# Performance work log

Measured on AMD Instinct MI355X. Metric: run time of the kernel, lower is better.

The kernel has to match this reference:

```python
import jax, jax.numpy as jnp
import numpy as np

B, CIN, H, W = 4, 1024, 64, 64
PLANES = 256
K = 3
DIL = 2
PAD = DIL * (K - 1) // 2  # = 2
EPS = 1e-5


def setup_inputs() -> dict:
    key = jax.random.key(0)
    ks = jax.random.split(key, 16)
    d = {}
    d['x'] = jax.random.normal(ks[0], (B, CIN, H, W), dtype=jnp.float32)
    # conv1: 1x1, inplanes->planes, no bias
    d['w1'] = jax.random.normal(ks[1], (PLANES, CIN), dtype=jnp.float32) * 0.02
    d['gamma1'] = jnp.ones((PLANES,), jnp.float32)
    d['beta1'] = jnp.zeros((PLANES,), jnp.float32)
    d['mean1'] = jax.random.normal(ks[2], (PLANES,), dtype=jnp.float32) * 0.1
    d['var1'] = jax.random.uniform(ks[3], (PLANES,), minval=0.5, maxval=1.5, dtype=jnp.float32)
    # deform_offset: 3x3 conv planes->18, with bias
    d['woff'] = jax.random.normal(ks[4], (18, PLANES, K, K), dtype=jnp.float32) * 0.01
    d['boff'] = jnp.zeros((18,), jnp.float32)
    # conv2 (deformable): 3x3 planes->planes, with bias
    d['w2'] = jax.random.normal(ks[5], (PLANES, PLANES, K, K), dtype=jnp.float32) * 0.02
    d['bconv2'] = jnp.zeros((PLANES,), jnp.float32)
    d['gamma2'] = jnp.ones((PLANES,), jnp.float32)
    d['beta2'] = jnp.zeros((PLANES,), jnp.float32)
    d['mean2'] = jax.random.normal(ks[6], (PLANES,), dtype=jnp.float32) * 0.1
    d['var2'] = jax.random.uniform(ks[7], (PLANES,), minval=0.5, maxval=1.5, dtype=jnp.float32)
    # conv3: 1x1 planes->planes*4, no bias
    d['w3'] = jax.random.normal(ks[8], (PLANES * 4, PLANES), dtype=jnp.float32) * 0.02
    d['gamma3'] = jnp.ones((PLANES * 4,), jnp.float32)
    d['beta3'] = jnp.zeros((PLANES * 4,), jnp.float32)
    d['mean3'] = jax.random.normal(ks[9], (PLANES * 4,), dtype=jnp.float32) * 0.1
    d['var3'] = jax.random.uniform(ks[10], (PLANES * 4,), minval=0.5, maxval=1.5, dtype=jnp.float32)
    return d


def _bn(x, gamma, beta, mean, var):
    # inference-mode BatchNorm over channel dim (NCHW)
    inv = jax.lax.rsqrt(var + EPS)
    return (x - mean[:, None, None]) * (inv * gamma)[:, None, None] + beta[:, None, None]


def _deform_conv(x, offset, w, b):
    # x: [B,C,H,W]; offset: [B,18,H,W] ordered (dy,dx) per kernel tap; w: [O,C,3,3]
    Bn, C, Hh, Ww = x.shape
    off = offset.reshape(Bn, K * K, 2, Hh, Ww)
    off_y, off_x = off[:, :, 0], off[:, :, 1]          # [B,9,H,W]
    kk = jnp.arange(K * K)
    base_y = (kk // K) * DIL - PAD                      # [9]
    base_x = (kk % K) * DIL - PAD
    ys = jnp.arange(Hh, dtype=x.dtype)
    xs = jnp.arange(Ww, dtype=x.dtype)
    py = base_y.astype(x.dtype)[None, :, None, None] + ys[None, None, :, None] + off_y
    px = base_x.astype(x.dtype)[None, :, None, None] + xs[None, None, None, :] + off_x

    def sample_one(img, py1, px1):
        # img [C,H,W]; py1/px1 [9,H,W] -> [C,9,H,W] bilinear with zero padding
        y0 = jnp.floor(py1)
        x0 = jnp.floor(px1)
        wy = py1 - y0
        wx = px1 - x0

        def gather(yc, xc):
            yi = yc.astype(jnp.int32)
            xi = xc.astype(jnp.int32)
            valid = ((yi >= 0) & (yi < Hh) & (xi >= 0) & (xi < Ww)).astype(img.dtype)
            yi = jnp.clip(yi, 0, Hh - 1)
            xi = jnp.clip(xi, 0, Ww - 1)
            return img[:, yi, xi] * valid[None]

        v00 = gather(y0, x0)
        v01 = gather(y0, x0 + 1)
        v10 = gather(y0 + 1, x0)
        v11 = gather(y0 + 1, x0 + 1)
        return (v00 * ((1 - wy) * (1 - wx))[None] + v01 * ((1 - wy) * wx)[None]
                + v10 * (wy * (1 - wx))[None] + v11 * (wy * wx)[None])

    sampled = jax.vmap(sample_one)(x, py, px)           # [B,C,9,H,W]
    out = jnp.einsum('bckhw,ock->bohw', sampled, w.reshape(w.shape[0], C, K * K))
    return out + b[None, :, None, None]


def reference(x, w1, gamma1, beta1, mean1, var1, woff, boff, w2, bconv2,
              gamma2, beta2, mean2, var2, w3, gamma3, beta3, mean3, var3):
    residual = x
    out = jnp.einsum('bchw,oc->bohw', x, w1)            # conv1 1x1
    out = jax.nn.relu(_bn(out, gamma1, beta1, mean1, var1))
    offset = jax.lax.conv_general_dilated(
        out, woff, window_strides=(1, 1), padding=((PAD, PAD), (PAD, PAD)),
        rhs_dilation=(DIL, DIL), dimension_numbers=('NCHW', 'OIHW', 'NCHW'))
    offset = offset + boff[None, :, None, None]
    out = _deform_conv(out, offset, w2, bconv2)
    out = jax.nn.relu(_bn(out, gamma2, beta2, mean2, var2))
    out = jnp.einsum('bchw,oc->bohw', out, w3)          # conv3 1x1
    out = _bn(out, gamma3, beta3, mean3, var3)
    return jax.nn.relu(out + residual)
```

## Files before the change

### kernel.cpp

```cpp
#include <hip/hip_runtime.h>

#define EPS_BN 1e-5f

typedef __bf16 bf16x8 __attribute__((ext_vector_type(8)));
typedef float f32x4 __attribute__((ext_vector_type(4)));

__device__ __forceinline__ unsigned short f2bf(float f) {
  union { float f; unsigned u; } v; v.f = f;
  unsigned r = v.u + 0x7fffu + ((v.u >> 16) & 1u);
  return (unsigned short)(r >> 16);
}
__device__ __forceinline__ float bf2f(unsigned short h) {
  union { unsigned u; float f; } v; v.u = ((unsigned)h) << 16;
  return v.f;
}

__global__ __launch_bounds__(256) void prep_all(
    const float* __restrict__ w1, const float* __restrict__ w2, const float* __restrict__ woff,
    const float* __restrict__ w3,
    const float* g1, const float* b1, const float* m1, const float* v1,
    const float* g2, const float* b2, const float* m2, const float* v2, const float* bconv2,
    const float* g3, const float* b3, const float* m3, const float* v3,
    unsigned short* __restrict__ w1b, unsigned short* __restrict__ w2r,
    uint4* __restrict__ act1Pz, unsigned short* __restrict__ wob,
    unsigned short* __restrict__ w3b, float* __restrict__ shift3,
    float* s1, float* h1, float* s2, float* h2) {
  int bid = blockIdx.x, tid = threadIdx.x;
  if (bid < 1024) {
    int i = bid * 256 + tid;
    w1b[i] = f2bf(w1[i]);
  } else if (bid < 3328) {
    int i = (bid - 1024) * 256 + tid;
    int o = i / 2304, r = i % 2304;
    int kk = r / 256, c = r % 256;
    w2r[i] = f2bf(w2[(size_t)o * 2304 + c * 9 + kk]);
  } else if (bid < 5640) {
    int i = (bid - 3328) * 256 + tid;
    if (i < 591872) act1Pz[i] = uint4{0, 0, 0, 0};
  } else if (bid < 5928) {
    int i = (bid - 5640) * 256 + tid;
    int o = i / 2304, r = i % 2304;
    int kk = r / 256, c = r % 256;
    wob[i] = (o < 18) ? f2bf(woff[(size_t)o * 2304 + c * 9 + kk]) : (unsigned short)0;
  } else if (bid < 6952) {
    int i = (bid - 5928) * 256 + tid;
    int o = i >> 8;
    float sc = rsqrtf(v3[o] + EPS_BN) * g3[o];
    w3b[i] = f2bf(w3[i] * sc);
  } else if (bid < 6956) {
    int c = (bid - 6952) * 256 + tid;
    float sc = rsqrtf(v3[c] + EPS_BN) * g3[c];
    shift3[c] = b3[c] - m3[c] * sc;
  } else {
    int c = tid;
    float sc1 = rsqrtf(v1[c] + EPS_BN) * g1[c];
    s1[c] = sc1; h1[c] = b1[c] - m1[c] * sc1;
    float sc2 = rsqrtf(v2[c] + EPS_BN) * g2[c];
    s2[c] = sc2; h2[c] = b2[c] + (bconv2[c] - m2[c]) * sc2;
  }
}

__global__ __launch_bounds__(256) void gemm1_x(
    const float* __restrict__ x, const unsigned short* __restrict__ Bm,
    unsigned short* __restrict__ part, int KH) {
  __shared__ __align__(16) char blob[16896];
  __shared__ __align__(16) unsigned short sA1[4096];
  __shared__ __align__(16) unsigned short sB1[4096];
  unsigned short* sA0 = (unsigned short*)blob;
  unsigned short* sB0 = (unsigned short*)(blob + 8192);
  float* tbuf = (float*)blob;
  int tid = threadIdx.x, lane = tid & 63, wv = tid >> 6;
  int z = blockIdx.z;
  int m0 = blockIdx.y * 128, n0 = blockIdx.x * 128;
  f32x4 acc[4][4] = {};
  int rowB = tid >> 2, kcolB = (tid & 3) * 8;
  int px = tid & 127, c16 = (tid >> 7) * 16;
  int bb = m0 >> 12, p0 = m0 & 4095;
  const float* xa = x + (size_t)bb * 4194304 + (size_t)c16 * 4096 + (p0 + px);
  int wm = wv & 1, wn = wv >> 1;
  int lane15 = lane & 15, quad8 = (lane >> 4) * 8, quad = lane >> 4;

  float va[16];

#define G1_ISSUE_A(K0)                                                                    \
  {                                                                                       \
    const float* xp = xa + (size_t)(K0) * 4096;                                           \
    _Pragma("unroll") for (int j = 0; j < 16; ++j) va[j] = xp[(size_t)j * 4096];          \
  }

#define G1_ISSUE_B(DB, K0)                                                                \
  {                                                                                       \
    _Pragma("unroll") for (int r = 0; r < 2; ++r) {                                       \
      const unsigned short* gp = Bm + (size_t)(n0 + r * 64 + rowB) * 1024 + (K0) + kcolB; \
      __builtin_amdgcn_global_load_lds((const __attribute__((address_space(1))) void*)gp, \
          (__attribute__((address_space(3))) void*)&(DB)[r * 2048 + wv * 512], 16, 0, 0); \
    }                                                                                     \
  }

#define G1_CVT_WRITE(DA)                                                                  \
  {                                                                                       \
    unsigned o8[8];                                                                       \
    _Pragma("unroll") for (int j = 0; j < 8; ++j)                                         \
      o8[j] = (unsigned)f2bf(va[2 * j]) | ((unsigned)f2bf(va[2 * j + 1]) << 16);          \
    unsigned short* wp = (DA) + px * 32 + c16;                                            \
    *(uint4*)(wp) = uint4{o8[0], o8[1], o8[2], o8[3]};                                    \
    *(uint4*)(wp + 8) = uint4{o8[4], o8[5], o8[6], o8[7]};                                \
  }

#define G1_COMPUTE(DA, DB)                                                                \
  {                                                                                       \
    bf16x8 afr[4], bfr[4];                                                                \
    _Pragma("unroll") for (int mi = 0; mi < 4; ++mi)                                      \
      afr[mi] = *(const bf16x8*)&(DA)[(wm * 64 + mi * 16 + lane15) * 32 + quad8];         \
    _Pragma("unroll") for (int ni = 0; ni < 4; ++ni)                                      \
      bfr[ni] = *(const bf16x8*)&(DB)[(wn * 64 + ni * 16 + lane15) * 32 + quad8];         \
    _Pragma("unroll") for (int mi = 0; mi < 4; ++mi)                                      \
      _Pragma("unroll") for (int ni = 0; ni < 4; ++ni)                                    \
        acc[mi][ni] =                                                                     \
            __builtin_amdgcn_mfma_f32_16x16x32_bf16(afr[mi], bfr[ni], acc[mi][ni], 0, 0, 0); \
  }

#define G1_BODY(K0, AC, BC, AN, BN_)                                                      \
  {                                                                                       \
    G1_ISSUE_A(K0);                                                                       \
    G1_ISSUE_B(BN_, K0);                                                                  \
    asm volatile("s_waitcnt vmcnt(18)" ::: "memory");                                     \
    asm volatile("s_waitcnt lgkmcnt(0)" ::: "memory");                                    \
    __builtin_amdgcn_s_barrier();                                                         \
    G1_COMPUTE(AC, BC);                                                                   \
    asm volatile("s_waitcnt vmcnt(2)" ::: "memory");                                      \
    G1_CVT_WRITE(AN);                                                                     \
    __builtin_amdgcn_s_barrier();                                                         \
  }

  int kbase = z * KH;
  int nst = KH >> 5;
  G1_ISSUE_A(kbase);
  G1_ISSUE_B(sB0, kbase);
  asm volatile("s_waitcnt vmcnt(2)" ::: "memory");
  G1_CVT_WRITE(sA0);
  for (int t = 0; t + 2 < nst; t += 2) {
    G1_BODY(kbase + (t + 1) * 32, sA0, sB0, sA1, sB1);
    G1_BODY(kbase + (t + 2) * 32, sA1, sB1, sA0, sB0);
  }
  G1_BODY(kbase + (nst - 1) * 32, sA0, sB0, sA1, sB1);
  asm volatile("s_waitcnt vmcnt(0)" ::: "memory");
  asm volatile("s_waitcnt lgkmcnt(0)" ::: "memory");
  __builtin_amdgcn_s_barrier();
  G1_COMPUTE(sA1, sB1);
#undef G1_ISSUE_A
#undef G1_ISSUE_B
#undef G1_CVT_WRITE
#undef G1_COMPUTE
#undef G1_BODY

  unsigned short* outH = part + (size_t)z * 16384 * 256;
  int trow = tid >> 3;
  int tcol16 = (tid & 7) * 16;
  int growBase = m0 + (trow >> 4) * 64 + (trow & 15);
#pragma unroll
  for (int mi = 0; mi < 4; ++mi) {
    __syncthreads();
#pragma unroll
    for (int ni = 0; ni < 4; ++ni)
#pragma unroll
      for (int reg = 0; reg < 4; ++reg)
        tbuf[(wm * 16 + quad * 4 + reg) * 132 + wn * 64 + ni * 16 + lane15] = acc[mi][ni][reg];
    __syncthreads();
    int gr = growBase + mi * 16;
    const float* lp = &tbuf[trow * 132 + tcol16];
    unsigned o[8];
#pragma unroll
    for (int j = 0; j < 8; ++j)
      o[j] = (unsigned)f2bf(lp[2 * j]) | ((unsigned)f2bf(lp[2 * j + 1]) << 16);
    unsigned short* op = outH + (size_t)gr * 256 + n0 + tcol16;
    *(uint4*)(op) = uint4{o[0], o[1], o[2], o[3]};
    *(uint4*)(op + 8) = uint4{o[4], o[5], o[6], o[7]};
  }
}

__global__ __launch_bounds__(256) void gemm_split(
    const unsigned short* __restrict__ A, const unsigned short* __restrict__ Bm,
    unsigned short* __restrict__ part, int M, int N, int K, int KH) {
  __shared__ __align__(16) char blob[16896];
  __shared__ __align__(16) unsigned short sA1[4096];
  __shared__ __align__(16) unsigned short sB1[4096];
  unsigned short* sA0 = (unsigned short*)blob;
  unsigned short* sB0 = (unsigned short*)(blob + 8192);
  float* tbuf = (float*)blob;
  int tid = threadIdx.x, lane = tid & 63, wv = tid >> 6;
  int z = blockIdx.z;
  int m0 = blockIdx.y * 128, n0 = blockIdx.x * 128;
  f32x4 acc[4][4] = {};
  int rowA = tid >> 2;
  int kcol = (tid & 3) * 8;
  int wm = wv & 1, wn = wv >> 1;
  int lane15 = lane & 15, quad8 = (lane >> 4) * 8, quad = lane >> 4;

#define GS_STAGE(dA, dB, K0)                                                              \
  {                                                                                       \
    int k0_ = (K0);                                                                       \
    _Pragma("unroll") for (int r = 0; r < 2; ++r) {                                       \
      const unsigned short* gp = A + (size_t)(m0 + r * 64 + rowA) * K + k0_ + kcol;       \
      __builtin_amdgcn_global_load_lds((const __attribute__((address_space(1))) void*)gp, \
          (__attribute__((address_space(3))) void*)&(dA)[r * 2048 + wv * 512], 16, 0, 0); \
    }                                                                                     \
    _Pragma("unroll") for (int r = 0; r < 2; ++r) {                                       \
      const unsigned short* gp = Bm + (size_t)(n0 + r * 64 + rowA) * K + k0_ + kcol;      \
      __builtin_amdgcn_global_load_lds((const __attribute__((address_space(1))) void*)gp, \
          (__attribute__((address_space(3))) void*)&(dB)[r * 2048 + wv * 512], 16, 0, 0); \
    }                                                                                     \
  }

#define GS_COMPUTE(dA, dB)                                                                \
  {                                                                                       \
    bf16x8 afr[4], bfr[4];                                                                \
    _Pragma("unroll") for (int mi = 0; mi < 4; ++mi)                                      \
      afr[mi] = *(const bf16x8*)&(dA)[(wm * 64 + mi * 16 + lane15) * 32 + quad8];         \
    _Pragma("unroll") for (int ni = 0; ni < 4; ++ni)                                      \
      bfr[ni] = *(const bf16x8*)&(dB)[(wn * 64 + ni * 16 + lane15) * 32 + quad8];         \
    _Pragma("unroll") for (int mi = 0; mi < 4; ++mi)                                      \
      _Pragma("unroll") for (int ni = 0; ni < 4; ++ni)                                    \
        acc[mi][ni] =                                                                     \
            __builtin_amdgcn_mfma_f32_16x16x32_bf16(afr[mi], bfr[ni], acc[mi][ni], 0, 0, 0); \
  }

  int kbase = z * KH;
  int nst = KH >> 5;
  GS_STAGE(sA0, sB0, kbase);
  for (int t = 0; t < nst; t += 2) {
    GS_STAGE(sA1, sB1, kbase + (t + 1) * 32);
    asm volatile("s_waitcnt vmcnt(4)" ::: "memory");
    __builtin_amdgcn_s_barrier();
    GS_COMPUTE(sA0, sB0);
    __builtin_amdgcn_s_barrier();
    if (t + 2 < nst) {
      GS_STAGE(sA0, sB0, kbase + (t + 2) * 32);
      asm volatile("s_waitcnt vmcnt(4)" ::: "memory");
    } else {
      asm volatile("s_waitcnt vmcnt(0)" ::: "memory");
    }
    __builtin_amdgcn_s_barrier();
    GS_COMPUTE(sA1, sB1);
    __builtin_amdgcn_s_barrier();
  }
#undef GS_STAGE
#undef GS_COMPUTE

  unsigned short* outH = part + (size_t)z * M * N;
  int trow = tid >> 3;
  int tcol16 = (tid & 7) * 16;
  int growBase = m0 + (trow >> 4) * 64 + (trow & 15);
#pragma unroll
  for (int mi = 0; mi < 4; ++mi) {
    __syncthreads();
#pragma unroll
    for (int ni = 0; ni < 4; ++ni)
#pragma unroll
      for (int reg = 0; reg < 4; ++reg)
        tbuf[(wm * 16 + quad * 4 + reg) * 132 + wn * 64 + ni * 16 + lane15] = acc[mi][ni][reg];
    __syncthreads();
    int gr = growBase + mi * 16;
    const float* lp = &tbuf[trow * 132 + tcol16];
    unsigned o[8];
#pragma unroll
    for (int j = 0; j < 8; ++j)
      o[j] = (unsigned)f2bf(lp[2 * j]) | ((unsigned)f2bf(lp[2 * j + 1]) << 16);
    unsigned short* op = outH + (size_t)gr * 256 + n0 + tcol16;
    *(uint4*)(op) = uint4{o[0], o[1], o[2], o[3]};
    *(uint4*)(op + 8) = uint4{o[4], o[5], o[6], o[7]};
  }
}

template <int NS, int PAD>
__global__ __launch_bounds__(256) void epi_bn(const unsigned short* __restrict__ part,
                                              const float* __restrict__ scale,
                                              const float* __restrict__ shift,
                                              unsigned short* __restrict__ outT,
                                              unsigned short* __restrict__ outP) {
  int gid = blockIdx.x * 256 + threadIdx.x;
  int row = gid >> 5, c0 = (gid & 31) * 8;
  float v[8] = {};
#pragma unroll
  for (int s = 0; s < NS; ++s) {
    uint4 q = *(const uint4*)(part + (size_t)s * 16384 * 256 + (size_t)row * 256 + c0);
    unsigned u[4] = {q.x, q.y, q.z, q.w};
#pragma unroll
    for (int j = 0; j < 4; ++j) {
      v[2 * j]     += bf2f((unsigned short)(u[j] & 0xffffu));
      v[2 * j + 1] += bf2f((unsigned short)(u[j] >> 16));
    }
  }
  float sc[8], sh[8];
  *(float4*)&sc[0] = *(const float4*)(scale + c0); *(float4*)&sc[4] = *(const float4*)(scale + c0 + 4);
  *(float4*)&sh[0] = *(const float4*)(shift + c0); *(float4*)&sh[4] = *(const float4*)(shift + c0 + 4);
  unsigned o[4];
#pragma unroll
  for (int j = 0; j < 4; ++j) {
    float lo = fmaxf(v[2 * j] * sc[2 * j] + sh[2 * j], 0.f);
    float hi = fmaxf(v[2 * j + 1] * sc[2 * j + 1] + sh[2 * j + 1], 0.f);
    o[j] = (unsigned)f2bf(lo) | ((unsigned)f2bf(hi) << 16);
  }
  uint4 pk{o[0], o[1], o[2], o[3]};
  *(uint4*)(outT + (size_t)row * 256 + c0) = pk;
  if constexpr (PAD) {
    int bb = row >> 12, p = row & 4095;
    *(uint4*)(outP + (((size_t)(bb * 68) + (p >> 6) + 2) * 68 + (p & 63) + 2) * 256 + c0) = pk;
  }
}

__global__ __launch_bounds__(256) void gemm_res(
    const unsigned short* __restrict__ A, const unsigned short* __restrict__ Bm,
    float* __restrict__ outp, const float* __restrict__ shift3,
    const float* __restrict__ resid, int M, int N, int K, long bStrideB, long bStrideOut) {
  __shared__ __align__(16) char blob[16896];
  __shared__ __align__(16) unsigned short sA1[4096];
  __shared__ __align__(16) unsigned short sB1[4096];
  unsigned short* sA0 = (unsigned short*)blob;
  unsigned short* sB0 = (unsigned short*)(blob + 8192);
  float* tbuf = (float*)blob;
  int tid = threadIdx.x, lane = tid & 63, wv = tid >> 6;
  int z = blockIdx.z;
  const unsigned short* Bz = Bm + (size_t)z * bStrideB;
  int m0 = blockIdx.y * 128, n0 = blockIdx.x * 128;
  f32x4 acc[4][4] = {};
  int rowA = tid >> 2;
  int kcol = (tid & 3) * 8;
  int wm = wv & 1, wn = wv >> 1;
  int lane15 = lane & 15, quad8 = (lane >> 4) * 8, quad = lane >> 4;

#define GR_STAGE(dA, dB, K0)                                                              \
  {                                                                                       \
    int k0_ = (K0);                                                                       \
    _Pragma("unroll") for (int r = 0; r < 2; ++r) {                                       \
      const unsigned short* gp = A + (size_t)(m0 + r * 64 + rowA) * K + k0_ + kcol;       \
      __builtin_amdgcn_global_load_lds((const __attribute__((address_space(1))) void*)gp, \
          (__attribute__((address_space(3))) void*)&(dA)[r * 2048 + wv * 512], 16, 0, 0); \
    }                                                                                     \
    _Pragma("unroll") for (int r = 0; r < 2; ++r) {                                       \
      const unsigned short* gp = Bz + (size_t)(n0 + r * 64 + rowA) * K + k0_ + kcol;      \
      __builtin_amdgcn_global_load_lds((const __attribute__((address_space(1))) void*)gp, \
          (__attribute__((address_space(3))) void*)&(dB)[r * 2048 + wv * 512], 16, 0, 0); \
    }                                                                                     \
  }

#define GR_COMPUTE(dA, dB)                                                                \
  {                                                                                       \
    bf16x8 afr[4], bfr[4];                                                                \
    _Pragma("unroll") for (int mi = 0; mi < 4; ++mi)                                      \
      afr[mi] = *(const bf16x8*)&(dA)[(wm * 64 + mi * 16 + lane15) * 32 + quad8];         \
    _Pragma("unroll") for (int ni = 0; ni < 4; ++ni)                                      \
      bfr[ni] = *(const bf16x8*)&(dB)[(wn * 64 + ni * 16 + lane15) * 32 + quad8];         \
    _Pragma("unroll") for (int mi = 0; mi < 4; ++mi)                                      \
      _Pragma("unroll") for (int ni = 0; ni < 4; ++ni)                                    \
        acc[mi][ni] =                                                                     \
            __builtin_amdgcn_mfma_f32_16x16x32_bf16(afr[mi], bfr[ni], acc[mi][ni], 0, 0, 0); \
  }

  int nst = K >> 5;
  GR_STAGE(sA0, sB0, 0);
  for (int t = 0; t < nst; t += 2) {
    GR_STAGE(sA1, sB1, (t + 1) * 32);
    asm volatile("s_waitcnt vmcnt(4)" ::: "memory");
    __builtin_amdgcn_s_barrier();
    GR_COMPUTE(sA0, sB0);
    __builtin_amdgcn_s_barrier();
    if (t + 2 < nst) {
      GR_STAGE(sA0, sB0, (t + 2) * 32);
      asm volatile("s_waitcnt vmcnt(4)" ::: "memory");
    } else {
      asm volatile("s_waitcnt vmcnt(0)" ::: "memory");
    }
    __builtin_amdgcn_s_barrier();
    GR_COMPUTE(sA1, sB1);
    __builtin_amdgcn_s_barrier();
  }
#undef GR_STAGE
#undef GR_COMPUTE

  float* outF = outp + (size_t)z * bStrideOut;
  const float* res = resid + (size_t)z * bStrideOut;
  int trow = tid >> 3;
  int tcol = (tid & 7) * 4;
  int growBase = m0 + (trow >> 4) * 64 + (trow & 15);
#pragma unroll
  for (int mi = 0; mi < 4; ++mi) {
    __syncthreads();
#pragma unroll
    for (int ni = 0; ni < 4; ++ni)
#pragma unroll
      for (int reg = 0; reg < 4; ++reg)
        tbuf[(wm * 16 + quad * 4 + reg) * 132 + wn * 64 + ni * 16 + lane15] = acc[mi][ni][reg];
    __syncthreads();
    int gr = growBase + mi * 16;
    float sh = shift3[gr];
    const float* rp = res + (size_t)gr * N + n0 + tcol;
    float* op = outF + (size_t)gr * N + n0 + tcol;
    const float* lp = &tbuf[trow * 132 + tcol];
#pragma unroll
    for (int j = 0; j < 4; ++j) {
      float4 rv = *(const float4*)(rp + j * 32);
      float4 lv = *(const float4*)(lp + j * 32);
      float4 ov;
      ov.x = fmaxf(lv.x + sh + rv.x, 0.f);
      ov.y = fmaxf(lv.y + sh + rv.y, 0.f);
      ov.z = fmaxf(lv.z + sh + rv.z, 0.f);
      ov.w = fmaxf(lv.w + sh + rv.w, 0.f);
      *(float4*)(op + j * 32) = ov;
    }
  }
}

__global__ __launch_bounds__(256) void off_gemm(const unsigned short* __restrict__ actP,
                                                const unsigned short* __restrict__ wob,
                                                const float* __restrict__ boff,
                                                float* __restrict__ offsP) {
  __shared__ __align__(16) unsigned short sA0[4096];
  __shared__ __align__(16) unsigned short sB0[2048];
  __shared__ __align__(16) unsigned short sA1[4096];
  __shared__ __align__(16) unsigned short sB1[2048];
  int tid = threadIdx.x, lane = tid & 63, wv = tid >> 6;
  int m0 = blockIdx.x * 64;
  int lane15 = lane & 15, quad8 = (lane >> 4) * 8;
  int rowA = tid >> 3;
  int kc = (tid & 7) * 8;

  const unsigned short* baseA[2];
#pragma unroll
  for (int r = 0; r < 2; ++r) {
    int row = m0 + r * 32 + rowA;
    int b = row >> 12, p = row & 4095;
    baseA[r] = actP + (((size_t)(b * 68) + (p >> 6) + 2) * 68 + (p & 63) + 2) * 256 + kc;
  }
  const unsigned short* baseB = wob + (size_t)rowA * 2304 + kc;

  f32x4 acc[2] = {};

#define OG_STAGE(dA, dB, S)                                                               \
  {                                                                                       \
    int s_ = (S); int kk_ = s_ >> 2; int c0_ = (s_ & 3) * 64;                             \
    long shift_ = (long)(((kk_ / 3) * 2 - 2) * 68 + ((kk_ % 3) * 2 - 2));                 \
    _Pragma("unroll") for (int r = 0; r < 2; ++r) {                                       \
      const unsigned short* gp = baseA[r] + shift_ * 256 + c0_;                           \
      __builtin_amdgcn_global_load_lds((const __attribute__((address_space(1))) void*)gp, \
          (__attribute__((address_space(3))) void*)&(dA)[r * 2048 + wv * 512], 16, 0, 0); \
    }                                                                                     \
    {                                                                                     \
      const unsigned short* gp = baseB + kk_ * 256 + c0_;                                 \
      __builtin_amdgcn_global_load_lds((const __attribute__((address_space(1))) void*)gp, \
          (__attribute__((address_space(3))) void*)&(dB)[wv * 512], 16, 0, 0);            \
    }                                                                                     \
  }

#define OG_COMPUTE(dA, dB)                                                                \
  {                                                                                       \
    bf16x8 afr[2], bfr[2][2];                                                             \
    _Pragma("unroll") for (int kq = 0; kq < 2; ++kq) {                                    \
      afr[kq] = *(const bf16x8*)&(dA)[(wv * 16 + lane15) * 64 + kq * 32 + quad8];         \
      _Pragma("unroll") for (int ni = 0; ni < 2; ++ni)                                    \
        bfr[kq][ni] = *(const bf16x8*)&(dB)[(ni * 16 + lane15) * 64 + kq * 32 + quad8];   \
    }                                                                                     \
    _Pragma("unroll") for (int kq = 0; kq < 2; ++kq)                                      \
      _Pragma("unroll") for (int ni = 0; ni < 2; ++ni)                                    \
        acc[ni] = __builtin_amdgcn_mfma_f32_16x16x32_bf16(afr[kq], bfr[kq][ni], acc[ni], 0, 0, 0); \
  }

  OG_STAGE(sA0, sB0, 0);
  for (int s = 0; s < 36; s += 2) {
    OG_STAGE(sA1, sB1, s + 1);
    asm volatile("s_waitcnt vmcnt(3)" ::: "memory");
    __builtin_amdgcn_s_barrier();
    OG_COMPUTE(sA0, sB0);
    __builtin_amdgcn_s_barrier();
    if (s + 2 < 36) {
      OG_STAGE(sA0, sB0, s + 2);
      asm volatile("s_waitcnt vmcnt(3)" ::: "memory");
    } else {
      asm volatile("s_waitcnt vmcnt(0)" ::: "memory");
    }
    __builtin_amdgcn_s_barrier();
    OG_COMPUTE(sA1, sB1);
    __builtin_amdgcn_s_barrier();
  }
#undef OG_STAGE
#undef OG_COMPUTE

#pragma unroll
  for (int ni = 0; ni < 2; ++ni) {
    int o = ni * 16 + lane15;
    if (o < 18) {
      float bo = boff[o];
#pragma unroll
      for (int reg = 0; reg < 4; ++reg) {
        int row = m0 + wv * 16 + (lane >> 4) * 4 + reg;
        offsP[(size_t)row * 18 + o] = acc[ni][reg] + bo;
      }
    }
  }
}

__global__ __launch_bounds__(256) void deform_sample(const unsigned short* __restrict__ act1T,
                                                     const float* __restrict__ offsP,
                                                     unsigned short* __restrict__ S) {
  int g = threadIdx.x >> 5, t = threadIdx.x & 31;
  int idx = blockIdx.x * 8 + g;
  int b = idx >> 12, p = idx & 4095;
  int h = p >> 6, w = p & 63;
  const unsigned short* actb = act1T + (size_t)b * 4096 * 256 + t * 8;
  unsigned short* Sp = S + (size_t)idx * 2304 + t * 8;
  float ov = (t < 18) ? offsP[(size_t)idx * 18 + t] : 0.f;
#pragma unroll
  for (int kk = 0; kk < 9; ++kk) {
    float offy = __shfl(ov, 2 * kk, 32);
    float offx = __shfl(ov, 2 * kk + 1, 32);
    float py = (float)(h + (kk / 3) * 2 - 2) + offy;
    float px = (float)(w + (kk % 3) * 2 - 2) + offx;
    float fy = floorf(py), fx = floorf(px);
    int y0 = (int)fy, x0 = (int)fx;
    float wy = py - fy, wx = px - fx;
    bool yv0 = (y0 >= 0 && y0 < 64), yv1 = (y0 >= -1 && y0 < 63);
    bool xv0 = (x0 >= 0 && x0 < 64), xv1 = (x0 >= -1 && x0 < 63);
    const unsigned short* cb = actb + (y0 * 64 + x0) * 256;
    uint4 q00{0,0,0,0}, q01{0,0,0,0}, q10{0,0,0,0}, q11{0,0,0,0};
    if (yv0 && xv0) q00 = *(const uint4*)(cb);
    if (yv0 && xv1) q01 = *(const uint4*)(cb + 256);
    if (yv1 && xv0) q10 = *(const uint4*)(cb + 64 * 256);
    if (yv1 && xv1) q11 = *(const uint4*)(cb + 64 * 256 + 256);
    float w00 = (1.f - wy) * (1.f - wx), w01 = (1.f - wy) * wx;
    float w10 = wy * (1.f - wx), w11 = wy * wx;
    unsigned u00[4] = {q00.x, q00.y, q00.z, q00.w};
    unsigned u01[4] = {q01.x, q01.y, q01.z, q01.w};
    unsigned u10[4] = {q10.x, q10.y, q10.z, q10.w};
    unsigned u11[4] = {q11.x, q11.y, q11.z, q11.w};
    unsigned out[4];
#pragma unroll
    for (int j = 0; j < 4; ++j) {
      float lo = bf2f((unsigned short)(u00[j] & 0xffffu)) * w00 +
                 bf2f((unsigned short)(u01[j] & 0xffffu)) * w01 +
                 bf2f((unsigned short)(u10[j] & 0xffffu)) * w10 +
                 bf2f((unsigned short)(u11[j] & 0xffffu)) * w11;
      float hi = bf2f((unsigned short)(u00[j] >> 16)) * w00 +
                 bf2f((unsigned short)(u01[j] >> 16)) * w01 +
                 bf2f((unsigned short)(u10[j] >> 16)) * w10 +
                 bf2f((unsigned short)(u11[j] >> 16)) * w11;
      out[j] = (unsigned)f2bf(lo) | ((unsigned)f2bf(hi) << 16);
    }
    *(uint4*)(Sp + kk * 256) = uint4{out[0], out[1], out[2], out[3]};
  }
}

extern "C" void kernel_launch(void* const* d_in, const int* in_sizes, int n_in,
                              void* d_out, int out_size, void* d_ws, size_t ws_size,
                              hipStream_t stream) {
  const float* x      = (const float*)d_in[0];
  const float* w1     = (const float*)d_in[1];
  const float* gamma1 = (const float*)d_in[2];
  const float* beta1  = (const float*)d_in[3];
  const float* mean1  = (const float*)d_in[4];
  const float* var1   = (const float*)d_in[5];
  const float* woff   = (const float*)d_in[6];
  const float* boff   = (const float*)d_in[7];
  const float* w2     = (const float*)d_in[8];
  const float* bconv2 = (const float*)d_in[9];
  const float* gamma2 = (const float*)d_in[10];
  const float* beta2  = (const float*)d_in[11];
  const float* mean2  = (const float*)d_in[12];
  const float* var2   = (const float*)d_in[13];
  const float* w3     = (const float*)d_in[14];
  const float* gamma3 = (const float*)d_in[15];
  const float* beta3  = (const float*)d_in[16];
  const float* mean3  = (const float*)d_in[17];
  const float* var3   = (const float*)d_in[18];

  char* ws = (char*)d_ws;
  unsigned short* act1T = (unsigned short*)(ws + 33554432);
  unsigned short* act2T = (unsigned short*)(ws + 41943040);
  unsigned short* S     = (unsigned short*)(ws + 50331648);
  float*          offs  = (float*)(ws + 125829120);
  unsigned short* w1b   = (unsigned short*)(ws + 127008768);
  unsigned short* w2r   = (unsigned short*)(ws + 127533056);
  unsigned short* w3b   = (unsigned short*)(ws + 128712704);
  float*          bnS1  = (float*)(ws + 129236992);
  float*          bnH1  = (float*)(ws + 129238016);
  float*          bnS2  = (float*)(ws + 129239040);
  float*          bnH2  = (float*)(ws + 129240064);
  float*          shift3= (float*)(ws + 129241088);
  unsigned short* act1P = S;
  unsigned short* part1 = (unsigned short*)(ws + 62914560);
  unsigned short* part2 = (unsigned short*)ws;
  unsigned short* wob   = act2T;

  prep_all<<<6957, 256, 0, stream>>>(w1, w2, woff, w3,
                                     gamma1, beta1, mean1, var1,
                                     gamma2, beta2, mean2, var2, bconv2,
                                     gamma3, beta3, mean3, var3,
                                     w1b, w2r, (uint4*)act1P, wob, w3b, shift3,
                                     bnS1, bnH1, bnS2, bnH2);

  gemm1_x<<<dim3(2, 128, 2), 256, 0, stream>>>(x, w1b, part1, 512);
  epi_bn<2, 1><<<2048, 256, 0, stream>>>(part1, bnS1, bnH1, act1T, act1P);

  off_gemm<<<256, 256, 0, stream>>>(act1P, wob, boff, offs);
  deform_sample<<<dim3(2048), 256, 0, stream>>>(act1T, offs, S);

  gemm_split<<<dim3(2, 128, 2), 256, 0, stream>>>(S, w2r, part2, 16384, 256, 2304, 1152);
  epi_bn<2, 0><<<2048, 256, 0, stream>>>(part2, bnS2, bnH2, act2T, nullptr);

  gemm_res<<<dim3(32, 8, 4), 256, 0, stream>>>(w3b, act2T, (float*)d_out, shift3, x,
                                               1024, 4096, 256, 4096L * 256, 4194304L);
}
```

Before: 280.5 us.

## XOR-swizzle LDS tiles in GEMM kernels and widen gemm_split K-tile

Applies an XOR swizzle on the 16-byte chunk index when writing and reading LDS tiles in gemm1_x, gemm_split and gemm_res, to remove bank conflicts on the bf16x8 fragment loads. gemm_split also moves from a 32-wide to a 64-wide K tile, doubling its LDS buffers and halving the number of barrier-separated stages. The larger LDS footprint in gemm_split may lower occupancy, and the swizzle adds a little index arithmetic per load.

```diff
diff --git a/kernel.cpp b/kernel.cpp
--- a/kernel.cpp
+++ b/kernel.cpp
@@ -73,12 +73,14 @@
   int z = blockIdx.z;
   int m0 = blockIdx.y * 128, n0 = blockIdx.x * 128;
   f32x4 acc[4][4] = {};
-  int rowB = tid >> 2, kcolB = (tid & 3) * 8;
-  int px = tid & 127, c16 = (tid >> 7) * 16;
+  int rowB = tid >> 2;
+  int kcolBs = (((tid & 3) ^ (rowB & 3))) * 8;
+  int px = tid & 127, chalf = tid >> 7;
+  int s0w = (chalf * 2) ^ (px & 3), s1w = (chalf * 2 + 1) ^ (px & 3);
   int bb = m0 >> 12, p0 = m0 & 4095;
-  const float* xa = x + (size_t)bb * 4194304 + (size_t)c16 * 4096 + (p0 + px);
+  const float* xa = x + (size_t)bb * 4194304 + (size_t)(chalf * 16) * 4096 + (p0 + px);
   int wm = wv & 1, wn = wv >> 1;
-  int lane15 = lane & 15, quad8 = (lane >> 4) * 8, quad = lane >> 4;
+  int lane15 = lane & 15, quad = lane >> 4, l3 = lane & 3;
 
   float va[16];
 
@@ -91,7 +93,7 @@
 #define G1_ISSUE_B(DB, K0)                                                                \
   {                                                                                       \
     _Pragma("unroll") for (int r = 0; r < 2; ++r) {                                       \
-      const unsigned short* gp = Bm + (size_t)(n0 + r * 64 + rowB) * 1024 + (K0) + kcolB; \
+      const unsigned short* gp = Bm + (size_t)(n0 + r * 64 + rowB) * 1024 + (K0) + kcolBs;\
       __builtin_amdgcn_global_load_lds((const __attribute__((address_space(1))) void*)gp, \
           (__attribute__((address_space(3))) void*)&(DB)[r * 2048 + wv * 512], 16, 0, 0); \
     }                                                                                     \
@@ -102,18 +104,17 @@
     unsigned o8[8];                                                                       \
     _Pragma("unroll") for (int j = 0; j < 8; ++j)                                         \
       o8[j] = (unsigned)f2bf(va[2 * j]) | ((unsigned)f2bf(va[2 * j + 1]) << 16);          \
-    unsigned short* wp = (DA) + px * 32 + c16;                                            \
-    *(uint4*)(wp) = uint4{o8[0], o8[1], o8[2], o8[3]};                                    \
-    *(uint4*)(wp + 8) = uint4{o8[4], o8[5], o8[6], o8[7]};                                \
+    *(uint4*)((DA) + px * 32 + s0w * 8) = uint4{o8[0], o8[1], o8[2], o8[3]};              \
+    *(uint4*)((DA) + px * 32 + s1w * 8) = uint4{o8[4], o8[5], o8[6], o8[7]};              \
   }
 
 #define G1_COMPUTE(DA, DB)                                                                \
   {                                                                                       \
     bf16x8 afr[4], bfr[4];                                                                \
     _Pragma("unroll") for (int mi = 0; mi < 4; ++mi)                                      \
-      afr[mi] = *(const bf16x8*)&(DA)[(wm * 64 + mi * 16 + lane15) * 32 + quad8];         \
+      afr[mi] = *(const bf16x8*)&(DA)[(wm * 64 + mi * 16 + lane15) * 32 + (quad ^ l3) * 8]; \
     _Pragma("unroll") for (int ni = 0; ni < 4; ++ni)                                      \
-      bfr[ni] = *(const bf16x8*)&(DB)[(wn * 64 + ni * 16 + lane15) * 32 + quad8];         \
+      bfr[ni] = *(const bf16x8*)&(DB)[(wn * 64 + ni * 16 + lane15) * 32 + (quad ^ l3) * 8]; \
     _Pragma("unroll") for (int mi = 0; mi < 4; ++mi)                                      \
       _Pragma("unroll") for (int ni = 0; ni < 4; ++ni)                                    \
         acc[mi][ni] =                                                                     \
@@ -182,31 +183,31 @@
 __global__ __launch_bounds__(256) void gemm_split(
     const unsigned short* __restrict__ A, const unsigned short* __restrict__ Bm,
     unsigned short* __restrict__ part, int M, int N, int K, int KH) {
-  __shared__ __align__(16) char blob[16896];
-  __shared__ __align__(16) unsigned short sA1[4096];
-  __shared__ __align__(16) unsigned short sB1[4096];
+  __shared__ __align__(16) char blob[32768];
+  __shared__ __align__(16) unsigned short sA1[8192];
+  __shared__ __align__(16) unsigned short sB1[8192];
   unsigned short* sA0 = (unsigned short*)blob;
-  unsigned short* sB0 = (unsigned short*)(blob + 8192);
+  unsigned short* sB0 = (unsigned short*)(blob + 16384);
   float* tbuf = (float*)blob;
   int tid = threadIdx.x, lane = tid & 63, wv = tid >> 6;
   int z = blockIdx.z;
   int m0 = blockIdx.y * 128, n0 = blockIdx.x * 128;
   f32x4 acc[4][4] = {};
-  int rowA = tid >> 2;
-  int kcol = (tid & 3) * 8;
+  int rowS = tid >> 3;
+  int colS = (((tid & 7) ^ (rowS & 7))) * 8;
   int wm = wv & 1, wn = wv >> 1;
-  int lane15 = lane & 15, quad8 = (lane >> 4) * 8, quad = lane >> 4;
+  int lane15 = lane & 15, quad = lane >> 4, l7 = lane & 7;
 
 #define GS_STAGE(dA, dB, K0)                                                              \
   {                                                                                       \
     int k0_ = (K0);                                                                       \
-    _Pragma("unroll") for (int r = 0; r < 2; ++r) {                                       \
-      const unsigned short* gp = A + (size_t)(m0 + r * 64 + rowA) * K + k0_ + kcol;       \
+    _Pragma("unroll") for (int r = 0; r < 4; ++r) {                                       \
+      const unsigned short* gp = A + (size_t)(m0 + r * 32 + rowS) * K + k0_ + colS;       \
       __builtin_amdgcn_global_load_lds((const __attribute__((address_space(1))) void*)gp, \
           (__attribute__((address_space(3))) void*)&(dA)[r * 2048 + wv * 512], 16, 0, 0); \
     }                                                                                     \
-    _Pragma("unroll") for (int r = 0; r < 2; ++r) {                                       \
-      const unsigned short* gp = Bm + (size_t)(n0 + r * 64 + rowA) * K + k0_ + kcol;      \
+    _Pragma("unroll") for (int r = 0; r < 4; ++r) {                                       \
+      const unsigned short* gp = Bm + (size_t)(n0 + r * 32 + rowS) * K + k0_ + colS;      \
       __builtin_amdgcn_global_load_lds((const __attribute__((address_space(1))) void*)gp, \
           (__attribute__((address_space(3))) void*)&(dB)[r * 2048 + wv * 512], 16, 0, 0); \
     }                                                                                     \
@@ -214,29 +215,33 @@
 
 #define GS_COMPUTE(dA, dB)                                                                \
   {                                                                                       \
-    bf16x8 afr[4], bfr[4];                                                                \
-    _Pragma("unroll") for (int mi = 0; mi < 4; ++mi)                                      \
-      afr[mi] = *(const bf16x8*)&(dA)[(wm * 64 + mi * 16 + lane15) * 32 + quad8];         \
-    _Pragma("unroll") for (int ni = 0; ni < 4; ++ni)                                      \
-      bfr[ni] = *(const bf16x8*)&(dB)[(wn * 64 + ni * 16 + lane15) * 32 + quad8];         \
-    _Pragma("unroll") for (int mi = 0; mi < 4; ++mi)                                      \
+    _Pragma("unroll") for (int kq = 0; kq < 2; ++kq) {                                    \
+      bf16x8 afr[4], bfr[4];                                                              \
+      _Pragma("unroll") for (int mi = 0; mi < 4; ++mi)                                    \
+        afr[mi] = *(const bf16x8*)&(dA)[(wm * 64 + mi * 16 + lane15) * 64 +               \
+                                        ((kq * 4 + quad) ^ l7) * 8];                      \
       _Pragma("unroll") for (int ni = 0; ni < 4; ++ni)                                    \
-        acc[mi][ni] =                                                                     \
-            __builtin_amdgcn_mfma_f32_16x16x32_bf16(afr[mi], bfr[ni], acc[mi][ni], 0, 0, 0); \
+        bfr[ni] = *(const bf16x8*)&(dB)[(wn * 64 + ni * 16 + lane15) * 64 +               \
+                                        ((kq * 4 + quad) ^ l7) * 8];                      \
+      _Pragma("unroll") for (int mi = 0; mi < 4; ++mi)                                    \
+        _Pragma("unroll") for (int ni = 0; ni < 4; ++ni)                                  \
+          acc[mi][ni] =                                                                   \
+              __builtin_amdgcn_mfma_f32_16x16x32_bf16(afr[mi], bfr[ni], acc[mi][ni], 0, 0, 0); \
+    }                                                                                     \
   }
 
   int kbase = z * KH;
-  int nst = KH >> 5;
+  int nst = KH >> 6;
   GS_STAGE(sA0, sB0, kbase);
   for (int t = 0; t < nst; t += 2) {
-    GS_STAGE(sA1, sB1, kbase + (t + 1) * 32);
-    asm volatile("s_waitcnt vmcnt(4)" ::: "memory");
+    GS_STAGE(sA1, sB1, kbase + (t + 1) * 64);
+    asm volatile("s_waitcnt vmcnt(8)" ::: "memory");
     __builtin_amdgcn_s_barrier();
     GS_COMPUTE(sA0, sB0);
     __builtin_amdgcn_s_barrier();
     if (t + 2 < nst) {
-      GS_STAGE(sA0, sB0, kbase + (t + 2) * 32);
-      asm volatile("s_waitcnt vmcnt(4)" ::: "memory");
+      GS_STAGE(sA0, sB0, kbase + (t + 2) * 64);
+      asm volatile("s_waitcnt vmcnt(8)" ::: "memory");
     } else {
       asm volatile("s_waitcnt vmcnt(0)" ::: "memory");
     }
@@ -325,20 +330,20 @@
   int m0 = blockIdx.y * 128, n0 = blockIdx.x * 128;
   f32x4 acc[4][4] = {};
   int rowA = tid >> 2;
-  int kcol = (tid & 3) * 8;
+  int kcolS = (((tid & 3) ^ (rowA & 3))) * 8;
   int wm = wv & 1, wn = wv >> 1;
-  int lane15 = lane & 15, quad8 = (lane >> 4) * 8, quad = lane >> 4;
+  int lane15 = lane & 15, quad = lane >> 4, l3 = lane & 3;
 
 #define GR_STAGE(dA, dB, K0)                                                              \
   {                                                                                       \
     int k0_ = (K0);                                                                       \
     _Pragma("unroll") for (int r = 0; r < 2; ++r) {                                       \
-      const unsigned short* gp = A + (size_t)(m0 + r * 64 + rowA) * K + k0_ + kcol;       \
+      const unsigned short* gp = A + (size_t)(m0 + r * 64 + rowA) * K + k0_ + kcolS;      \
       __builtin_amdgcn_global_load_lds((const __attribute__((address_space(1))) void*)gp, \
           (__attribute__((address_space(3))) void*)&(dA)[r * 2048 + wv * 512], 16, 0, 0); \
     }                                                                                     \
     _Pragma("unroll") for (int r = 0; r < 2; ++r) {                                       \
-      const unsigned short* gp = Bz + (size_t)(n0 + r * 64 + rowA) * K + k0_ + kcol;      \
+      const unsigned short* gp = Bz + (size_t)(n0 + r * 64 + rowA) * K + k0_ + kcolS;     \
       __builtin_amdgcn_global_load_lds((const __attribute__((address_space(1))) void*)gp, \
           (__attribute__((address_space(3))) void*)&(dB)[r * 2048 + wv * 512], 16, 0, 0); \
     }                                                                                     \
@@ -348,9 +353,9 @@
   {                                                                                       \
     bf16x8 afr[4], bfr[4];                                                                \
     _Pragma("unroll") for (int mi = 0; mi < 4; ++mi)                                      \
-      afr[mi] = *(const bf16x8*)&(dA)[(wm * 64 + mi * 16 + lane15) * 32 + quad8];         \
+      afr[mi] = *(const bf16x8*)&(dA)[(wm * 64 + mi * 16 + lane15) * 32 + (quad ^ l3) * 8]; \
     _Pragma("unroll") for (int ni = 0; ni < 4; ++ni)                                      \
-      bfr[ni] = *(const bf16x8*)&(dB)[(wn * 64 + ni * 16 + lane15) * 32 + quad8];         \
+      bfr[ni] = *(const bf16x8*)&(dB)[(wn * 64 + ni * 16 + lane15) * 32 + (quad ^ l3) * 8]; \
     _Pragma("unroll") for (int mi = 0; mi < 4; ++mi)                                      \
       _Pragma("unroll") for (int ni = 0; ni < 4; ++ni)                                    \
         acc[mi][ni] =                                                                     \
```

New measurement: 276.5 us. Within noise of the previous version (-1.4%).

## XOR-swizzle GEMM LDS tiles and raise split-K from 2 to 4

Applied to the files above, without the earlier changes.

Applies an XOR swizzle to the 16-byte chunk index in the LDS A/B tiles of the three MFMA GEMM kernels, on both the global-to-LDS writes and the fragment reads, to cut LDS bank conflicts. It also doubles the split-K factor for gemm1_x and gemm_split (KH halved, grid z 4) with matching epi_bn<4> reductions, adding blocks for occupancy. The cost is twice the partial-sum traffic and a heavier epilogue reduction. The part buffers must be large enough for four partial slices.

```diff
diff --git a/kernel.cpp b/kernel.cpp
--- a/kernel.cpp
+++ b/kernel.cpp
@@ -73,12 +73,16 @@
   int z = blockIdx.z;
   int m0 = blockIdx.y * 128, n0 = blockIdx.x * 128;
   f32x4 acc[4][4] = {};
-  int rowB = tid >> 2, kcolB = (tid & 3) * 8;
-  int px = tid & 127, c16 = (tid >> 7) * 16;
+  int rowB = tid >> 2;
+  int kcolBs = ((tid & 3) ^ ((tid >> 3) & 3)) * 8;
+  int px = tid & 127, chalf = tid >> 7;
+  int akey = (px >> 1) & 3;
+  int s0w = (chalf * 2) ^ akey, s1w = (chalf * 2 + 1) ^ akey;
   int bb = m0 >> 12, p0 = m0 & 4095;
-  const float* xa = x + (size_t)bb * 4194304 + (size_t)c16 * 4096 + (p0 + px);
+  const float* xa = x + (size_t)bb * 4194304 + (size_t)(chalf * 16) * 4096 + (p0 + px);
   int wm = wv & 1, wn = wv >> 1;
-  int lane15 = lane & 15, quad8 = (lane >> 4) * 8, quad = lane >> 4;
+  int lane15 = lane & 15, quad = lane >> 4;
+  int rkey = (lane15 >> 1) & 3;
 
   float va[16];
 
@@ -91,7 +95,7 @@
 #define G1_ISSUE_B(DB, K0)                                                                \
   {                                                                                       \
     _Pragma("unroll") for (int r = 0; r < 2; ++r) {                                       \
-      const unsigned short* gp = Bm + (size_t)(n0 + r * 64 + rowB) * 1024 + (K0) + kcolB; \
+      const unsigned short* gp = Bm + (size_t)(n0 + r * 64 + rowB) * 1024 + (K0) + kcolBs;\
       __builtin_amdgcn_global_load_lds((const __attribute__((address_space(1))) void*)gp, \
           (__attribute__((address_space(3))) void*)&(DB)[r * 2048 + wv * 512], 16, 0, 0); \
     }                                                                                     \
@@ -102,18 +106,17 @@
     unsigned o8[8];                                                                       \
     _Pragma("unroll") for (int j = 0; j < 8; ++j)                                         \
       o8[j] = (unsigned)f2bf(va[2 * j]) | ((unsigned)f2bf(va[2 * j + 1]) << 16);          \
-    unsigned short* wp = (DA) + px * 32 + c16;                                            \
-    *(uint4*)(wp) = uint4{o8[0], o8[1], o8[2], o8[3]};                                    \
-    *(uint4*)(wp + 8) = uint4{o8[4], o8[5], o8[6], o8[7]};                                \
+    *(uint4*)((DA) + px * 32 + s0w * 8) = uint4{o8[0], o8[1], o8[2], o8[3]};              \
+    *(uint4*)((DA) + px * 32 + s1w * 8) = uint4{o8[4], o8[5], o8[6], o8[7]};              \
   }
 
 #define G1_COMPUTE(DA, DB)                                                                \
   {                                                                                       \
     bf16x8 afr[4], bfr[4];                                                                \
     _Pragma("unroll") for (int mi = 0; mi < 4; ++mi)                                      \
-      afr[mi] = *(const bf16x8*)&(DA)[(wm * 64 + mi * 16 + lane15) * 32 + quad8];         \
+      afr[mi] = *(const bf16x8*)&(DA)[(wm * 64 + mi * 16 + lane15) * 32 + (quad ^ rkey) * 8]; \
     _Pragma("unroll") for (int ni = 0; ni < 4; ++ni)                                      \
-      bfr[ni] = *(const bf16x8*)&(DB)[(wn * 64 + ni * 16 + lane15) * 32 + quad8];         \
+      bfr[ni] = *(const bf16x8*)&(DB)[(wn * 64 + ni * 16 + lane15) * 32 + (quad ^ rkey) * 8]; \
     _Pragma("unroll") for (int mi = 0; mi < 4; ++mi)                                      \
       _Pragma("unroll") for (int ni = 0; ni < 4; ++ni)                                    \
         acc[mi][ni] =                                                                     \
@@ -193,20 +196,21 @@
   int m0 = blockIdx.y * 128, n0 = blockIdx.x * 128;
   f32x4 acc[4][4] = {};
   int rowA = tid >> 2;
-  int kcol = (tid & 3) * 8;
+  int kcolS = ((tid & 3) ^ ((tid >> 3) & 3)) * 8;
   int wm = wv & 1, wn = wv >> 1;
-  int lane15 = lane & 15, quad8 = (lane >> 4) * 8, quad = lane >> 4;
+  int lane15 = lane & 15, quad = lane >> 4;
+  int rkey = (lane15 >> 1) & 3;
 
 #define GS_STAGE(dA, dB, K0)                                                              \
   {                                                                                       \
     int k0_ = (K0);                                                                       \
     _Pragma("unroll") for (int r = 0; r < 2; ++r) {                                       \
-      const unsigned short* gp = A + (size_t)(m0 + r * 64 + rowA) * K + k0_ + kcol;       \
+      const unsigned short* gp = A + (size_t)(m0 + r * 64 + rowA) * K + k0_ + kcolS;      \
       __builtin_amdgcn_global_load_lds((const __attribute__((address_space(1))) void*)gp, \
           (__attribute__((address_space(3))) void*)&(dA)[r * 2048 + wv * 512], 16, 0, 0); \
     }                                                                                     \
     _Pragma("unroll") for (int r = 0; r < 2; ++r) {                                       \
-      const unsigned short* gp = Bm + (size_t)(n0 + r * 64 + rowA) * K + k0_ + kcol;      \
+      const unsigned short* gp = Bm + (size_t)(n0 + r * 64 + rowA) * K + k0_ + kcolS;     \
       __builtin_amdgcn_global_load_lds((const __attribute__((address_space(1))) void*)gp, \
           (__attribute__((address_space(3))) void*)&(dB)[r * 2048 + wv * 512], 16, 0, 0); \
     }                                                                                     \
@@ -216,9 +220,9 @@
   {                                                                                       \
     bf16x8 afr[4], bfr[4];                                                                \
     _Pragma("unroll") for (int mi = 0; mi < 4; ++mi)                                      \
-      afr[mi] = *(const bf16x8*)&(dA)[(wm * 64 + mi * 16 + lane15) * 32 + quad8];         \
+      afr[mi] = *(const bf16x8*)&(dA)[(wm * 64 + mi * 16 + lane15) * 32 + (quad ^ rkey) * 8]; \
     _Pragma("unroll") for (int ni = 0; ni < 4; ++ni)                                      \
-      bfr[ni] = *(const bf16x8*)&(dB)[(wn * 64 + ni * 16 + lane15) * 32 + quad8];         \
+      bfr[ni] = *(const bf16x8*)&(dB)[(wn * 64 + ni * 16 + lane15) * 32 + (quad ^ rkey) * 8]; \
     _Pragma("unroll") for (int mi = 0; mi < 4; ++mi)                                      \
       _Pragma("unroll") for (int ni = 0; ni < 4; ++ni)                                    \
         acc[mi][ni] =                                                                     \
@@ -325,20 +329,21 @@
   int m0 = blockIdx.y * 128, n0 = blockIdx.x * 128;
   f32x4 acc[4][4] = {};
   int rowA = tid >> 2;
-  int kcol = (tid & 3) * 8;
+  int kcolS = ((tid & 3) ^ ((tid >> 3) & 3)) * 8;
   int wm = wv & 1, wn = wv >> 1;
-  int lane15 = lane & 15, quad8 = (lane >> 4) * 8, quad = lane >> 4;
+  int lane15 = lane & 15, quad = lane >> 4;
+  int rkey = (lane15 >> 1) & 3;
 
 #define GR_STAGE(dA, dB, K0)                                                              \
   {                                                                                       \
     int k0_ = (K0);                                                                       \
     _Pragma("unroll") for (int r = 0; r < 2; ++r) {                                       \
-      const unsigned short* gp = A + (size_t)(m0 + r * 64 + rowA) * K + k0_ + kcol;       \
+      const unsigned short* gp = A + (size_t)(m0 + r * 64 + rowA) * K + k0_ + kcolS;      \
       __builtin_amdgcn_global_load_lds((const __attribute__((address_space(1))) void*)gp, \
           (__attribute__((address_space(3))) void*)&(dA)[r * 2048 + wv * 512], 16, 0, 0); \
     }                                                                                     \
     _Pragma("unroll") for (int r = 0; r < 2; ++r) {                                       \
-      const unsigned short* gp = Bz + (size_t)(n0 + r * 64 + rowA) * K + k0_ + kcol;      \
+      const unsigned short* gp = Bz + (size_t)(n0 + r * 64 + rowA) * K + k0_ + kcolS;     \
       __builtin_amdgcn_global_load_lds((const __attribute__((address_space(1))) void*)gp, \
           (__attribute__((address_space(3))) void*)&(dB)[r * 2048 + wv * 512], 16, 0, 0); \
     }                                                                                     \
@@ -348,9 +353,9 @@
   {                                                                                       \
     bf16x8 afr[4], bfr[4];                                                                \
     _Pragma("unroll") for (int mi = 0; mi < 4; ++mi)                                      \
-      afr[mi] = *(const bf16x8*)&(dA)[(wm * 64 + mi * 16 + lane15) * 32 + quad8];         \
+      afr[mi] = *(const bf16x8*)&(dA)[(wm * 64 + mi * 16 + lane15) * 32 + (quad ^ rkey) * 8]; \
     _Pragma("unroll") for (int ni = 0; ni < 4; ++ni)                                      \
-      bfr[ni] = *(const bf16x8*)&(dB)[(wn * 64 + ni * 16 + lane15) * 32 + quad8];         \
+      bfr[ni] = *(const bf16x8*)&(dB)[(wn * 64 + ni * 16 + lane15) * 32 + (quad ^ rkey) * 8]; \
     _Pragma("unroll") for (int mi = 0; mi < 4; ++mi)                                      \
       _Pragma("unroll") for (int ni = 0; ni < 4; ++ni)                                    \
         acc[mi][ni] =                                                                     \
@@ -597,14 +602,14 @@
                                      w1b, w2r, (uint4*)act1P, wob, w3b, shift3,
                                      bnS1, bnH1, bnS2, bnH2);
 
-  gemm1_x<<<dim3(2, 128, 2), 256, 0, stream>>>(x, w1b, part1, 512);
-  epi_bn<2, 1><<<2048, 256, 0, stream>>>(part1, bnS1, bnH1, act1T, act1P);
+  gemm1_x<<<dim3(2, 128, 4), 256, 0, stream>>>(x, w1b, part1, 256);
+  epi_bn<4, 1><<<2048, 256, 0, stream>>>(part1, bnS1, bnH1, act1T, act1P);
 
   off_gemm<<<256, 256, 0, stream>>>(act1P, wob, boff, offs);
   deform_sample<<<dim3(2048), 256, 0, stream>>>(act1T, offs, S);
 
-  gemm_split<<<dim3(2, 128, 2), 256, 0, stream>>>(S, w2r, part2, 16384, 256, 2304, 1152);
-  epi_bn<2, 0><<<2048, 256, 0, stream>>>(part2, bnS2, bnH2, act2T, nullptr);
+  gemm_split<<<dim3(2, 128, 4), 256, 0, stream>>>(S, w2r, part2, 16384, 256, 2304, 576);
+  epi_bn<4, 0><<<2048, 256, 0, stream>>>(part2, bnS2, bnH2, act2T, nullptr);
 
   gemm_res<<<dim3(32, 8, 4), 256, 0, stream>>>(w3b, act2T, (float*)d_out, shift3, x,
                                                1024, 4096, 256, 4096L * 256, 4194304L);
```

New measurement: 291.4 us. +3.9%, slower.
